# Kernel optimization log

Measured on AMD Instinct MI355X. Metric: run time of the kernel, lower is better.

## Reference

```python
import jax, jax.numpy as jnp
import numpy as np

N, E = 50000, 800000
F_IN, H, C = 128, 8, 32  # hidden=256, heads=8 -> C=32
DROP_P = 0.6


def setup_inputs() -> dict:
    key = jax.random.key(0)
    ks = jax.random.split(key, 8)
    x = jax.random.normal(ks[0], (N, F_IN), dtype=jnp.float32)
    edge_index = jax.random.randint(ks[1], (2, E), 0, N, dtype=jnp.int64)
    # precomputed inverted-dropout masks (Bernoulli keep * 1/(1-p)), as passed via dp_mask args
    dp_mask = (jax.random.uniform(ks[2], (E, H)) > DROP_P).astype(jnp.float32) / (1.0 - DROP_P)
    dp_mask_self = (jax.random.uniform(ks[3], (N, H)) > DROP_P).astype(jnp.float32) / (1.0 - DROP_P)
    # learned parameters of GATConv
    W = jax.random.normal(ks[4], (F_IN, H * C), dtype=jnp.float32) * (1.0 / np.sqrt(F_IN))
    att_src = jax.random.normal(ks[5], (H, C), dtype=jnp.float32) * 0.1
    att_dst = jax.random.normal(ks[6], (H, C), dtype=jnp.float32) * 0.1
    bias = jnp.zeros((H * C,), dtype=jnp.float32)
    return {"x": x, "edge_index": edge_index, "dp_mask": dp_mask,
            "dp_mask_self": dp_mask_self, "W": W, "att_src": att_src,
            "att_dst": att_dst, "bias": bias}


def reference(x, edge_index, dp_mask, dp_mask_self, W, att_src, att_dst, bias):
    n = x.shape[0]
    h = (x @ W).reshape(n, H, C)                      # [N,H,C]
    a_src = jnp.sum(h * att_src, axis=-1)             # [N,H] source-side score
    a_dst = jnp.sum(h * att_dst, axis=-1)             # [N,H] dest-side score
    # flow='target_to_source': aggregate at edge_index[0], gather from edge_index[1]
    dst = edge_index[0]
    src = edge_index[1]
    e_alpha = jax.nn.leaky_relu(a_src[src] + a_dst[dst], 0.2)   # [E,H]
    s_alpha = jax.nn.leaky_relu(a_src + a_dst, 0.2)             # [N,H] self-loops
    seg = jnp.concatenate([dst, jnp.arange(n, dtype=dst.dtype)])
    alpha = jnp.concatenate([e_alpha, s_alpha], axis=0)         # [E+N,H]
    # segment softmax over each destination's neighborhood (incl. self-loop)
    m = jax.ops.segment_max(alpha, seg, num_segments=n)
    ex = jnp.exp(alpha - m[seg])
    denom = jax.ops.segment_sum(ex, seg, num_segments=n)
    p = ex / denom[seg]                                         # [E+N,H]
    # dropout on attention coefficients (masks passed in)
    p = p * jnp.concatenate([dp_mask, dp_mask_self], axis=0)
    msgs = jnp.concatenate([h[src], h], axis=0)                 # [E+N,H,C]
    out = jax.ops.segment_sum(p[:, :, None] * msgs, seg, num_segments=n)
    return out.reshape(n, H * C) + bias                         # concat heads + bias
```

## Files before the change

### kernel.cpp

```cpp
#include <hip/hip_runtime.h>

#define NN 50000
#define FIN 128
#define HC 256
#define NH 8
#define NE 800000
#define WROW 136
#define GEMMB 782
#define NBLK1 3907
#define OVFCAP 131072

typedef __attribute__((ext_vector_type(8))) short short8;
typedef __attribute__((ext_vector_type(4))) short short4v;
typedef __attribute__((ext_vector_type(4))) float floatx4;

__device__ __forceinline__ float bf2f(unsigned short u) {
    union { unsigned int i; float f; } v; v.i = ((unsigned int)u) << 16; return v.f;
}
__device__ __forceinline__ unsigned short f2bf(float f) {
    union { float f; unsigned int i; } v; v.f = f;
    unsigned int r = v.i + 0x7fffu + ((v.i >> 16) & 1u);
    return (unsigned short)(r >> 16);
}
__device__ __forceinline__ float lrelu(float x) { return x > 0.f ? x : 0.2f * x; }
__device__ __forceinline__ float ldf(const void* p, int f32, long long i) {
    return f32 ? ((const float*)p)[i] : bf2f(((const unsigned short*)p)[i]);
}
__device__ __forceinline__ int lde(const int* ei, int i64, long long i) {
    return i64 ? (int)((const long long*)ei)[i] : ei[i];
}
__device__ __forceinline__ float sel8(const float s[2][4], int t2, int rr) {
    float a0 = t2 ? s[1][0] : s[0][0];
    float a1 = t2 ? s[1][1] : s[0][1];
    float a2 = t2 ? s[1][2] : s[0][2];
    float a3 = t2 ? s[1][3] : s[0][3];
    return (rr == 0) ? a0 : ((rr == 1) ? a1 : ((rr == 2) ? a2 : a3));
}
__device__ __forceinline__ float blo(unsigned int u) {
    union { unsigned int i; float f; } v; v.i = u << 16; return v.f;
}
__device__ __forceinline__ float bhi(unsigned int u) {
    union { unsigned int i; float f; } v; v.i = u & 0xFFFF0000u; return v.f;
}
__device__ __forceinline__ float bperm(int addr, float v) {
    return __uint_as_float((unsigned int)__builtin_amdgcn_ds_bpermute(addr, (int)__float_as_uint(v)));
}

__global__ __launch_bounds__(256) void k_front(
        const void* __restrict__ x, const int* __restrict__ ei,
        const void* __restrict__ dpm, const void* __restrict__ W,
        const void* __restrict__ as_, const void* __restrict__ ad_,
        int* __restrict__ flags, unsigned short* __restrict__ h,
        float* __restrict__ a_src, float* __restrict__ a_dst,
        int* __restrict__ cnt, int* __restrict__ ovfcnt,
        unsigned int* __restrict__ bucket, int2* __restrict__ ovf, int cap) {
    __shared__ unsigned short lwt[128 * WROW];
    __shared__ int s_bad, s_nz;
    const int tid = threadIdx.x;
    const int b = blockIdx.x;

    if (tid == 0) { s_bad = 0; s_nz = 0; }
    __syncthreads();
    {
        unsigned int wv = ((const unsigned int*)dpm)[tid];
        if (wv != 0u && wv != 0x40200000u) atomicAdd(&s_bad, 1);
        if (((const unsigned int*)ei)[2 * tid + 1] != 0u) atomicAdd(&s_nz, 1);
    }
    __syncthreads();
    const int f32 = (s_bad == 0) ? 1 : 0;
    const int i64 = (s_nz == 0) ? 1 : 0;
    if (b == 0 && tid == 0) { flags[0] = f32; flags[1] = i64; }

    if (b < GEMMB) {
        const int ch = b & 1;
        const int rb = b >> 1;
        {
            const int lcol = tid & 127;
            const int col = ch * 128 + lcol;
            const int k0 = (tid >> 7) * 64;
            if (f32) {
                const float* wp = (const float*)W + col;
                for (int k = k0; k < k0 + 64; k++) lwt[lcol * WROW + k] = f2bf(wp[(long long)k * HC]);
            } else {
                const unsigned short* wp = (const unsigned short*)W + col;
                for (int k = k0; k < k0 + 64; k++) lwt[lcol * WROW + k] = wp[(long long)k * HC];
            }
        }
        __syncthreads();

        const int lane = tid & 63;
        const int wave = tid >> 6;
        const int lrow = lane & 15;
        const int quad = lane >> 4;
        const int row0w = rb * 128 + wave * 32;

        short8 a[2][4];
        #pragma unroll
        for (int t = 0; t < 2; t++)
            #pragma unroll
            for (int q = 0; q < 4; q++)
                #pragma unroll
                for (int j = 0; j < 8; j++) a[t][q][j] = 0;

        #pragma unroll
        for (int t = 0; t < 2; t++) {
            int row = row0w + t * 16 + lrow;
            if (row < NN) {
                if (f32) {
                    const float* xp = (const float*)x + (long long)row * FIN + quad * 8;
                    #pragma unroll
                    for (int q = 0; q < 4; q++) {
                        floatx4 u0 = *(const floatx4*)(xp + q * 32);
                        floatx4 u1 = *(const floatx4*)(xp + q * 32 + 4);
                        #pragma unroll
                        for (int j = 0; j < 4; j++) {
                            a[t][q][j]     = (short)f2bf(u0[j]);
                            a[t][q][j + 4] = (short)f2bf(u1[j]);
                        }
                    }
                } else {
                    const unsigned short* xp = (const unsigned short*)x + (long long)row * FIN + quad * 8;
                    #pragma unroll
                    for (int q = 0; q < 4; q++) a[t][q] = *(const short8*)(xp + q * 32);
                }
            }
        }

        float sS[2][4], sD[2][4];
        #pragma unroll 4
        for (int ct = 0; ct < 8; ct++) {
            if ((ct & 1) == 0) {
                #pragma unroll
                for (int t = 0; t < 2; t++)
                    #pragma unroll
                    for (int r = 0; r < 4; r++) { sS[t][r] = 0.f; sD[t][r] = 0.f; }
            }
            floatx4 acc0 = {0.f, 0.f, 0.f, 0.f};
            floatx4 acc1 = {0.f, 0.f, 0.f, 0.f};
            const unsigned short* wp = lwt + (ct * 16 + lrow) * WROW + quad * 8;
            #pragma unroll
            for (int q = 0; q < 4; q++) {
                short8 bb = *(const short8*)(wp + q * 32);
                acc0 = __builtin_amdgcn_mfma_f32_16x16x32_bf16(a[0][q], bb, acc0, 0, 0, 0);
                acc1 = __builtin_amdgcn_mfma_f32_16x16x32_bf16(a[1][q], bb, acc1, 0, 0, 0);
            }
            const int gcol = ch * 128 + ct * 16 + lrow;
            #pragma unroll
            for (int r = 0; r < 4; r++) {
                int orow = row0w + quad * 4 + r;
                if (orow < NN) h[(long long)orow * HC + gcol] = f2bf(acc0[r]);
                int orow1 = orow + 16;
                if (orow1 < NN) h[(long long)orow1 * HC + gcol] = f2bf(acc1[r]);
            }
            float tS = ldf(as_, f32, gcol);
            float tD = ldf(ad_, f32, gcol);
            #pragma unroll
            for (int r = 0; r < 4; r++) {
                sS[0][r] += acc0[r] * tS;  sS[1][r] += acc1[r] * tS;
                sD[0][r] += acc0[r] * tD;  sD[1][r] += acc1[r] * tD;
            }
            if (ct & 1) {
                #pragma unroll
                for (int m = 1; m <= 8; m <<= 1)
                    #pragma unroll
                    for (int t = 0; t < 2; t++)
                        #pragma unroll
                        for (int r = 0; r < 4; r++) {
                            sS[t][r] += __shfl_xor(sS[t][r], m);
                            sD[t][r] += __shfl_xor(sD[t][r], m);
                        }
                int hd = ch * 4 + (ct >> 1);
                if (lrow < 8) {
                    int t2 = lrow >> 2, rr = lrow & 3;
                    int row = row0w + t2 * 16 + quad * 4 + rr;
                    if (row < NN) a_src[row * NH + hd] = sel8(sS, t2, rr);
                } else {
                    int lr = lrow - 8;
                    int t2 = lr >> 2, rr = lr & 3;
                    int row = row0w + t2 * 16 + quad * 4 + rr;
                    if (row < NN) a_dst[row * NH + hd] = sel8(sD, t2, rr);
                }
            }
        }
    } else {
        int e = (b - GEMMB) * 256 + tid;
        int dst = lde(ei, i64, e);
        int src = lde(ei, i64, (long long)NE + e);
        unsigned int msk = 0;
        if (f32) {
            const floatx4* dp = (const floatx4*)((const float*)dpm + (long long)e * 8);
            floatx4 d0 = dp[0], d1 = dp[1];
            #pragma unroll
            for (int j = 0; j < 4; j++) {
                msk |= (d0[j] != 0.f ? 1u : 0u) << j;
                msk |= (d1[j] != 0.f ? 1u : 0u) << (4 + j);
            }
        } else {
            short8 dd = *(const short8*)((const unsigned short*)dpm + (long long)e * 8);
            #pragma unroll
            for (int j = 0; j < 8; j++) msk |= (dd[j] != 0 ? 1u : 0u) << j;
        }
        unsigned int entry = (unsigned int)src | (msk << 16);
        int pos = atomicAdd(&cnt[dst], 1);
        if (pos < cap) bucket[(long long)dst * cap + pos] = entry;
        else {
            int op = atomicAdd(ovfcnt, 1);
            if (op < OVFCAP) ovf[op] = make_int2(dst, (int)entry);
        }
    }
}

__global__ __launch_bounds__(256) void k_aggr(
        const int* __restrict__ cnt, const int* __restrict__ ovfcnt,
        const unsigned int* __restrict__ bucket, const int2* __restrict__ ovf,
        const float* __restrict__ a_src, const float* __restrict__ a_dst,
        const unsigned short* __restrict__ h, const void* __restrict__ dps,
        const int* __restrict__ flags, const void* __restrict__ bs_,
        void* __restrict__ out, int cap) {
    int node = blockIdx.x * 4 + (threadIdx.x >> 6);
    int lane = threadIdx.x & 63;
    if (node >= NN) return;
    const int unode = __builtin_amdgcn_readfirstlane(node);
    const int f32 = flags[0];
    int novf = *ovfcnt; novf = novf > OVFCAP ? OVFCAP : novf;
    int mn = cnt[unode]; mn = mn < cap ? mn : cap;
    const unsigned int* __restrict__ bp = bucket + (long long)unode * cap;

    const int hh = lane >> 3;
    const int e8 = lane & 7;
    const int badr = (lane & 56) << 2;
    const int cb = lane * 4;
    const float adst = a_dst[unode * NH + hh];

    float dnp = 0.f;
    float acc0 = 0.f, acc1 = 0.f, acc2 = 0.f, acc3 = 0.f;

    for (int j = 0; j < mn; j += 8) {
        unsigned int u0 = bp[j + 0], u1 = bp[j + 1], u2 = bp[j + 2], u3 = bp[j + 3],
                     u4 = bp[j + 4], u5 = bp[j + 5], u6 = bp[j + 6], u7 = bp[j + 7];

        int idx = j + e8;
        int idxc = idx < mn ? idx : mn - 1;
        unsigned int ue = bp[idxc];
        int esrc = (int)(ue & 0xFFFFu);
        float al = a_src[esrc * NH + hh] + adst;
        float w = __expf(fmaxf(al, 0.2f * al));
        w = idx < mn ? w : 0.f;
        dnp += w;
        float ws = ((ue >> (16 + hh)) & 1u) ? w : -w;

        #define GATW(K) float w##K = bperm(badr + 4 * K, ws);
        GATW(0) GATW(1) GATW(2) GATW(3) GATW(4) GATW(5) GATW(6) GATW(7)
        #undef GATW

        #define GATH(K) \
            const unsigned short* hp##K = h + \
                (((long long)(__builtin_amdgcn_readfirstlane((int)u##K) & 0xFFFF)) << 8); \
            uint2 v##K = make_uint2(0u, 0u); \
            if (w##K > 0.f) v##K = *(const uint2*)(hp##K + cb);
        GATH(0) GATH(1) GATH(2) GATH(3) GATH(4) GATH(5) GATH(6) GATH(7)
        #undef GATH

        #define MACC(K) { float p = w##K * 2.5f; \
            acc0 = fmaf(p, blo(v##K.x), acc0); acc1 = fmaf(p, bhi(v##K.x), acc1); \
            acc2 = fmaf(p, blo(v##K.y), acc2); acc3 = fmaf(p, bhi(v##K.y), acc3); }
        MACC(0) MACC(1) MACC(2) MACC(3) MACC(4) MACC(5) MACC(6) MACC(7)
        #undef MACC
    }

    dnp += __shfl_xor(dnp, 1);
    dnp += __shfl_xor(dnp, 2);
    dnp += __shfl_xor(dnp, 4);
    float dn = dnp;

    for (int i = 0; i < novf; i++) {
        int2 tv = ovf[i];
        if (tv.x == node) {
            unsigned int u = (unsigned int)tv.y;
            int src = (int)(u & 0xFFFFu);
            float w = __expf(lrelu(a_src[src * NH + hh] + adst));
            dn += w;
            if ((u >> (16 + hh)) & 1u) {
                uint2 hv = *(const uint2*)(h + ((long long)src << 8) + cb);
                float p = w * 2.5f;
                acc0 = fmaf(p, blo(hv.x), acc0); acc1 = fmaf(p, bhi(hv.x), acc1);
                acc2 = fmaf(p, blo(hv.y), acc2); acc3 = fmaf(p, bhi(hv.y), acc3);
            }
        }
    }
    {
        float wS = __expf(lrelu(a_src[unode * NH + hh] + adst));
        dn += wS;
        float pS = wS * ldf(dps, f32, (long long)unode * NH + hh);
        uint2 hv = *(const uint2*)(h + ((long long)unode << 8) + cb);
        acc0 = fmaf(pS, blo(hv.x), acc0); acc1 = fmaf(pS, bhi(hv.x), acc1);
        acc2 = fmaf(pS, blo(hv.y), acc2); acc3 = fmaf(pS, bhi(hv.y), acc3);
    }
    float inv = 1.0f / dn;
    float b0 = ldf(bs_, f32, cb + 0), b1 = ldf(bs_, f32, cb + 1);
    float b2 = ldf(bs_, f32, cb + 2), b3 = ldf(bs_, f32, cb + 3);
    if (f32) {
        floatx4 o = {acc0 * inv + b0, acc1 * inv + b1, acc2 * inv + b2, acc3 * inv + b3};
        *(floatx4*)((float*)out + (long long)node * HC + cb) = o;
    } else {
        short4v o;
        o[0] = (short)f2bf(acc0 * inv + b0);
        o[1] = (short)f2bf(acc1 * inv + b1);
        o[2] = (short)f2bf(acc2 * inv + b2);
        o[3] = (short)f2bf(acc3 * inv + b3);
        *(short4v*)((unsigned short*)out + (long long)node * HC + cb) = o;
    }
}

extern "C" void kernel_launch(void* const* d_in, const int* in_sizes, int n_in,
                              void* d_out, int out_size, void* d_ws, size_t ws_size,
                              hipStream_t stream) {
    const void* x       = d_in[0];
    const int*  ei      = (const int*)d_in[1];
    const void* dp_mask = d_in[2];
    const void* dp_self = d_in[3];
    const void* W       = d_in[4];
    const void* att_s   = d_in[5];
    const void* att_d   = d_in[6];
    const void* bias    = d_in[7];

    char* w = (char*)d_ws;
    unsigned short* h      = (unsigned short*)(w + 0);
    float*          a_src  = (float*)(w + 25600000);
    float*          a_dst  = (float*)(w + 27200000);
    int*            cnt    = (int*)(w + 28800000);
    int*            ovfcnt = (int*)(w + 29000000);
    int*            flags  = (int*)(w + 29000064);
    int2*           ovf    = (int2*)(w + 29000960);
    unsigned int*   bucket = (unsigned int*)(w + 30049536);

    long long avail = (long long)ws_size - 30049536LL - 256LL;
    int cap = (int)(avail / 200000LL);
    if (cap > 64) cap = 64;
    if (cap < 4) cap = 4;

    hipMemsetAsync(cnt, 0, 200960, stream);
    k_front<<<NBLK1, 256, 0, stream>>>(x, ei, dp_mask, W, att_s, att_d,
                                       flags, h, a_src, a_dst, cnt, ovfcnt, bucket, ovf, cap);
    k_aggr<<<NN / 4, 256, 0, stream>>>(cnt, ovfcnt, bucket, ovf, a_src, a_dst, h,
                                       dp_self, flags, bias, d_out, cap);
}
```

Baseline: 216.5 us.

## Pad edge counters, batch edge fill per block, and hoist neighbor gathers

Edge bucketing moves to the first 782 blocks, each handling 1024 edges, so the fill overlaps the GEMM blocks scheduled after it. Per-node counters are spaced 16 ints apart so atomics on nearby nodes no longer share a cache line. The bucket capacity becomes a power of two so indexing uses shifts. In aggregation, the eight row gathers are issued unconditionally before the weight computation, and each lane's entry is selected from registers instead of a second bucket load. This gives more memory parallelism at the cost of fetching rows that dropout will mask out.

Result: slower. 236.6 us (+9.3%).

```diff
diff --git a/kernel.cpp b/kernel.cpp
--- a/kernel.cpp
+++ b/kernel.cpp
@@ -6,9 +6,11 @@
 #define NH 8
 #define NE 800000
 #define WROW 136
+#define FILLB 782
 #define GEMMB 782
-#define NBLK1 3907
+#define NBLK1 1564
 #define OVFCAP 131072
+#define CSTR 16
 
 typedef __attribute__((ext_vector_type(8))) short short8;
 typedef __attribute__((ext_vector_type(4))) short short4v;
@@ -53,7 +55,8 @@
         int* __restrict__ flags, unsigned short* __restrict__ h,
         float* __restrict__ a_src, float* __restrict__ a_dst,
         int* __restrict__ cnt, int* __restrict__ ovfcnt,
-        unsigned int* __restrict__ bucket, int2* __restrict__ ovf, int cap) {
+        unsigned int* __restrict__ bucket, int2* __restrict__ ovf,
+        int cap, int capl2) {
     __shared__ unsigned short lwt[128 * WROW];
     __shared__ int s_bad, s_nz;
     const int tid = threadIdx.x;
@@ -71,9 +74,41 @@
     const int i64 = (s_nz == 0) ? 1 : 0;
     if (b == 0 && tid == 0) { flags[0] = f32; flags[1] = i64; }
 
-    if (b < GEMMB) {
-        const int ch = b & 1;
-        const int rb = b >> 1;
+    if (b < FILLB) {
+        const long long e0 = (long long)b * 1024 + tid;
+        #pragma unroll
+        for (int i = 0; i < 4; i++) {
+            long long e = e0 + i * 256;
+            if (e < NE) {
+                int dst = lde(ei, i64, e);
+                int src = lde(ei, i64, (long long)NE + e);
+                unsigned int msk = 0;
+                if (f32) {
+                    const floatx4* dp = (const floatx4*)((const float*)dpm + e * 8);
+                    floatx4 d0 = dp[0], d1 = dp[1];
+                    #pragma unroll
+                    for (int j = 0; j < 4; j++) {
+                        msk |= (d0[j] != 0.f ? 1u : 0u) << j;
+                        msk |= (d1[j] != 0.f ? 1u : 0u) << (4 + j);
+                    }
+                } else {
+                    short8 dd = *(const short8*)((const unsigned short*)dpm + e * 8);
+                    #pragma unroll
+                    for (int j = 0; j < 8; j++) msk |= (dd[j] != 0 ? 1u : 0u) << j;
+                }
+                unsigned int entry = (unsigned int)src | (msk << 16);
+                int pos = atomicAdd(&cnt[dst * CSTR], 1);
+                if (pos < cap) bucket[((long long)dst << capl2) + pos] = entry;
+                else {
+                    int op = atomicAdd(ovfcnt, 1);
+                    if (op < OVFCAP) ovf[op] = make_int2(dst, (int)entry);
+                }
+            }
+        }
+    } else {
+        const int bb = b - FILLB;
+        const int ch = bb & 1;
+        const int rb = bb >> 1;
         {
             const int lcol = tid & 127;
             const int col = ch * 128 + lcol;
@@ -140,9 +175,9 @@
             const unsigned short* wp = lwt + (ct * 16 + lrow) * WROW + quad * 8;
             #pragma unroll
             for (int q = 0; q < 4; q++) {
-                short8 bb = *(const short8*)(wp + q * 32);
-                acc0 = __builtin_amdgcn_mfma_f32_16x16x32_bf16(a[0][q], bb, acc0, 0, 0, 0);
-                acc1 = __builtin_amdgcn_mfma_f32_16x16x32_bf16(a[1][q], bb, acc1, 0, 0, 0);
+                short8 bb2 = *(const short8*)(wp + q * 32);
+                acc0 = __builtin_amdgcn_mfma_f32_16x16x32_bf16(a[0][q], bb2, acc0, 0, 0, 0);
+                acc1 = __builtin_amdgcn_mfma_f32_16x16x32_bf16(a[1][q], bb2, acc1, 0, 0, 0);
             }
             const int gcol = ch * 128 + ct * 16 + lrow;
             #pragma unroll
@@ -182,31 +217,6 @@
                 }
             }
         }
-    } else {
-        int e = (b - GEMMB) * 256 + tid;
-        int dst = lde(ei, i64, e);
-        int src = lde(ei, i64, (long long)NE + e);
-        unsigned int msk = 0;
-        if (f32) {
-            const floatx4* dp = (const floatx4*)((const float*)dpm + (long long)e * 8);
-            floatx4 d0 = dp[0], d1 = dp[1];
-            #pragma unroll
-            for (int j = 0; j < 4; j++) {
-                msk |= (d0[j] != 0.f ? 1u : 0u) << j;
-                msk |= (d1[j] != 0.f ? 1u : 0u) << (4 + j);
-            }
-        } else {
-            short8 dd = *(const short8*)((const unsigned short*)dpm + (long long)e * 8);
-            #pragma unroll
-            for (int j = 0; j < 8; j++) msk |= (dd[j] != 0 ? 1u : 0u) << j;
-        }
-        unsigned int entry = (unsigned int)src | (msk << 16);
-        int pos = atomicAdd(&cnt[dst], 1);
-        if (pos < cap) bucket[(long long)dst * cap + pos] = entry;
-        else {
-            int op = atomicAdd(ovfcnt, 1);
-            if (op < OVFCAP) ovf[op] = make_int2(dst, (int)entry);
-        }
     }
 }
 
@@ -216,15 +226,15 @@
         const float* __restrict__ a_src, const float* __restrict__ a_dst,
         const unsigned short* __restrict__ h, const void* __restrict__ dps,
         const int* __restrict__ flags, const void* __restrict__ bs_,
-        void* __restrict__ out, int cap) {
+        void* __restrict__ out, int cap, int capl2) {
     int node = blockIdx.x * 4 + (threadIdx.x >> 6);
     int lane = threadIdx.x & 63;
     if (node >= NN) return;
     const int unode = __builtin_amdgcn_readfirstlane(node);
     const int f32 = flags[0];
     int novf = *ovfcnt; novf = novf > OVFCAP ? OVFCAP : novf;
-    int mn = cnt[unode]; mn = mn < cap ? mn : cap;
-    const unsigned int* __restrict__ bp = bucket + (long long)unode * cap;
+    int mn = cnt[unode * CSTR]; mn = mn < cap ? mn : cap;
+    const unsigned int* __restrict__ bp = bucket + ((long long)unode << capl2);
 
     const int hh = lane >> 3;
     const int e8 = lane & 7;
@@ -239,9 +249,21 @@
         unsigned int u0 = bp[j + 0], u1 = bp[j + 1], u2 = bp[j + 2], u3 = bp[j + 3],
                      u4 = bp[j + 4], u5 = bp[j + 5], u6 = bp[j + 6], u7 = bp[j + 7];
 
+        #define GATH(K) \
+            const unsigned short* hp##K = h + \
+                (((long long)(__builtin_amdgcn_readfirstlane((int)u##K) & 0xFFFF)) << 8); \
+            uint2 v##K = *(const uint2*)(hp##K + cb);
+        GATH(0) GATH(1) GATH(2) GATH(3) GATH(4) GATH(5) GATH(6) GATH(7)
+        #undef GATH
+
+        unsigned int s0a = (e8 & 1) ? u1 : u0;
+        unsigned int s1a = (e8 & 1) ? u3 : u2;
+        unsigned int s2a = (e8 & 1) ? u5 : u4;
+        unsigned int s3a = (e8 & 1) ? u7 : u6;
+        unsigned int t0a = (e8 & 2) ? s1a : s0a;
+        unsigned int t1a = (e8 & 2) ? s3a : s2a;
+        unsigned int ue  = (e8 & 4) ? t1a : t0a;
         int idx = j + e8;
-        int idxc = idx < mn ? idx : mn - 1;
-        unsigned int ue = bp[idxc];
         int esrc = (int)(ue & 0xFFFFu);
         float al = a_src[esrc * NH + hh] + adst;
         float w = __expf(fmaxf(al, 0.2f * al));
@@ -249,23 +271,15 @@
         dnp += w;
         float ws = ((ue >> (16 + hh)) & 1u) ? w : -w;
 
-        #define GATW(K) float w##K = bperm(badr + 4 * K, ws);
-        GATW(0) GATW(1) GATW(2) GATW(3) GATW(4) GATW(5) GATW(6) GATW(7)
-        #undef GATW
-
-        #define GATH(K) \
-            const unsigned short* hp##K = h + \
-                (((long long)(__builtin_amdgcn_readfirstlane((int)u##K) & 0xFFFF)) << 8); \
-            uint2 v##K = make_uint2(0u, 0u); \
-            if (w##K > 0.f) v##K = *(const uint2*)(hp##K + cb);
-        GATH(0) GATH(1) GATH(2) GATH(3) GATH(4) GATH(5) GATH(6) GATH(7)
-        #undef GATH
-
-        #define MACC(K) { float p = w##K * 2.5f; \
-            acc0 = fmaf(p, blo(v##K.x), acc0); acc1 = fmaf(p, bhi(v##K.x), acc1); \
-            acc2 = fmaf(p, blo(v##K.y), acc2); acc3 = fmaf(p, bhi(v##K.y), acc3); }
-        MACC(0) MACC(1) MACC(2) MACC(3) MACC(4) MACC(5) MACC(6) MACC(7)
-        #undef MACC
+        #define CONS(K) { \
+            float wv = bperm(badr + 4 * K, ws); \
+            float p = fmaxf(wv, 0.f) * 2.5f; \
+            unsigned int gx = wv > 0.f ? v##K.x : 0u; \
+            unsigned int gy = wv > 0.f ? v##K.y : 0u; \
+            acc0 = fmaf(p, blo(gx), acc0); acc1 = fmaf(p, bhi(gx), acc1); \
+            acc2 = fmaf(p, blo(gy), acc2); acc3 = fmaf(p, bhi(gy), acc3); }
+        CONS(0) CONS(1) CONS(2) CONS(3) CONS(4) CONS(5) CONS(6) CONS(7)
+        #undef CONS
     }
 
     dnp += __shfl_xor(dnp, 1);
@@ -329,19 +343,19 @@
     float*          a_src  = (float*)(w + 25600000);
     float*          a_dst  = (float*)(w + 27200000);
     int*            cnt    = (int*)(w + 28800000);
-    int*            ovfcnt = (int*)(w + 29000000);
-    int*            flags  = (int*)(w + 29000064);
-    int2*           ovf    = (int2*)(w + 29000960);
-    unsigned int*   bucket = (unsigned int*)(w + 30049536);
-
-    long long avail = (long long)ws_size - 30049536LL - 256LL;
-    int cap = (int)(avail / 200000LL);
-    if (cap > 64) cap = 64;
-    if (cap < 4) cap = 4;
-
-    hipMemsetAsync(cnt, 0, 200960, stream);
+    int*            ovfcnt = (int*)(w + 32000000);
+    int*            flags  = (int*)(w + 32000064);
+    int2*           ovf    = (int2*)(w + 32000960);
+    unsigned int*   bucket = (unsigned int*)(w + 33049536);
+
+    long long avail = (long long)ws_size - 33049536LL - 512LL;
+    int cap = 64, capl2 = 6;
+    while (cap > 4 && (long long)cap * 200000LL > avail) { cap >>= 1; capl2--; }
+
+    hipMemsetAsync(cnt, 0, 3200128, stream);
     k_front<<<NBLK1, 256, 0, stream>>>(x, ei, dp_mask, W, att_s, att_d,
-                                       flags, h, a_src, a_dst, cnt, ovfcnt, bucket, ovf, cap);
+                                       flags, h, a_src, a_dst, cnt, ovfcnt, bucket, ovf,
+                                       cap, capl2);
     k_aggr<<<NN / 4, 256, 0, stream>>>(cnt, ovfcnt, bucket, ovf, a_src, a_dst, h,
-                                       dp_self, flags, bias, d_out, cap);
-}
+                                       dp_self, flags, bias, d_out, cap, capl2);
+}
```

## Split front kernel into separate edge-fill and GEMM kernels; reuse A tile across halves

Applied to the files above, without the earlier changes.

The fused front kernel, which mixed GEMM blocks and edge-bucketing blocks, becomes two kernels: k_fill scatters edges into per-destination buckets and k_gemm computes h and the attention scores. Each GEMM block now loads its x rows once and loops over both 128-column halves of W, halving the redundant x reads and bf16 conversions. The bucket capacity is rounded to a power of two so addressing uses shifts. In exchange the GEMM and the atomic-heavy fill no longer run concurrently, there is an extra launch, and the smaller bucket cap may push more edges into the overflow list.

Measured after the change: 230.0 us. +6.3%, slower.

```diff
diff --git a/kernel.cpp b/kernel.cpp
--- a/kernel.cpp
+++ b/kernel.cpp
@@ -6,8 +6,8 @@
 #define NH 8
 #define NE 800000
 #define WROW 136
-#define GEMMB 782
-#define NBLK1 3907
+#define FILLB 3125
+#define GEMMB 391
 #define OVFCAP 131072
 
 typedef __attribute__((ext_vector_type(8))) short short8;
@@ -46,19 +46,14 @@
     return __uint_as_float((unsigned int)__builtin_amdgcn_ds_bpermute(addr, (int)__float_as_uint(v)));
 }
 
-__global__ __launch_bounds__(256) void k_front(
-        const void* __restrict__ x, const int* __restrict__ ei,
-        const void* __restrict__ dpm, const void* __restrict__ W,
-        const void* __restrict__ as_, const void* __restrict__ ad_,
-        int* __restrict__ flags, unsigned short* __restrict__ h,
-        float* __restrict__ a_src, float* __restrict__ a_dst,
-        int* __restrict__ cnt, int* __restrict__ ovfcnt,
-        unsigned int* __restrict__ bucket, int2* __restrict__ ovf, int cap) {
-    __shared__ unsigned short lwt[128 * WROW];
+__global__ __launch_bounds__(256) void k_fill(
+        const int* __restrict__ ei, const void* __restrict__ dpm,
+        int* __restrict__ flags, int* __restrict__ cnt, int* __restrict__ ovfcnt,
+        unsigned int* __restrict__ bucket, int2* __restrict__ ovf,
+        int cap, int capl2) {
     __shared__ int s_bad, s_nz;
     const int tid = threadIdx.x;
     const int b = blockIdx.x;
-
     if (tid == 0) { s_bad = 0; s_nz = 0; }
     __syncthreads();
     {
@@ -71,9 +66,92 @@
     const int i64 = (s_nz == 0) ? 1 : 0;
     if (b == 0 && tid == 0) { flags[0] = f32; flags[1] = i64; }
 
-    if (b < GEMMB) {
-        const int ch = b & 1;
-        const int rb = b >> 1;
+    const long long e = (long long)b * 256 + tid;
+    int dst = lde(ei, i64, e);
+    int src = lde(ei, i64, (long long)NE + e);
+    unsigned int msk = 0;
+    if (f32) {
+        const floatx4* dp = (const floatx4*)((const float*)dpm + e * 8);
+        floatx4 d0 = dp[0], d1 = dp[1];
+        #pragma unroll
+        for (int j = 0; j < 4; j++) {
+            msk |= (d0[j] != 0.f ? 1u : 0u) << j;
+            msk |= (d1[j] != 0.f ? 1u : 0u) << (4 + j);
+        }
+    } else {
+        short8 dd = *(const short8*)((const unsigned short*)dpm + e * 8);
+        #pragma unroll
+        for (int j = 0; j < 8; j++) msk |= (dd[j] != 0 ? 1u : 0u) << j;
+    }
+    unsigned int entry = (unsigned int)src | (msk << 16);
+    int pos = atomicAdd(&cnt[dst], 1);
+    if (pos < cap) bucket[((long long)dst << capl2) + pos] = entry;
+    else {
+        int op = atomicAdd(ovfcnt, 1);
+        if (op < OVFCAP) ovf[op] = make_int2(dst, (int)entry);
+    }
+}
+
+__global__ __launch_bounds__(256) void k_gemm(
+        const void* __restrict__ x, const void* __restrict__ dpm,
+        const void* __restrict__ W,
+        const void* __restrict__ as_, const void* __restrict__ ad_,
+        unsigned short* __restrict__ h,
+        float* __restrict__ a_src, float* __restrict__ a_dst) {
+    __shared__ unsigned short lwt[128 * WROW];
+    __shared__ int s_bad;
+    const int tid = threadIdx.x;
+    const int b = blockIdx.x;
+    if (tid == 0) s_bad = 0;
+    __syncthreads();
+    {
+        unsigned int wv = ((const unsigned int*)dpm)[tid];
+        if (wv != 0u && wv != 0x40200000u) atomicAdd(&s_bad, 1);
+    }
+    __syncthreads();
+    const int f32 = (s_bad == 0) ? 1 : 0;
+
+    const int lane = tid & 63;
+    const int wave = tid >> 6;
+    const int lrow = lane & 15;
+    const int quad = lane >> 4;
+    const int row0w = b * 128 + wave * 32;
+
+    short8 a[2][4];
+    #pragma unroll
+    for (int t = 0; t < 2; t++)
+        #pragma unroll
+        for (int q = 0; q < 4; q++)
+            #pragma unroll
+            for (int j = 0; j < 8; j++) a[t][q][j] = 0;
+
+    #pragma unroll
+    for (int t = 0; t < 2; t++) {
+        int row = row0w + t * 16 + lrow;
+        if (row < NN) {
+            if (f32) {
+                const float* xp = (const float*)x + (long long)row * FIN + quad * 8;
+                #pragma unroll
+                for (int q = 0; q < 4; q++) {
+                    floatx4 u0 = *(const floatx4*)(xp + q * 32);
+                    floatx4 u1 = *(const floatx4*)(xp + q * 32 + 4);
+                    #pragma unroll
+                    for (int j = 0; j < 4; j++) {
+                        a[t][q][j]     = (short)f2bf(u0[j]);
+                        a[t][q][j + 4] = (short)f2bf(u1[j]);
+                    }
+                }
+            } else {
+                const unsigned short* xp = (const unsigned short*)x + (long long)row * FIN + quad * 8;
+                #pragma unroll
+                for (int q = 0; q < 4; q++) a[t][q] = *(const short8*)(xp + q * 32);
+            }
+        }
+    }
+
+    #pragma unroll
+    for (int ch = 0; ch < 2; ch++) {
+        if (ch) __syncthreads();
         {
             const int lcol = tid & 127;
             const int col = ch * 128 + lcol;
@@ -87,44 +165,6 @@
             }
         }
         __syncthreads();
-
-        const int lane = tid & 63;
-        const int wave = tid >> 6;
-        const int lrow = lane & 15;
-        const int quad = lane >> 4;
-        const int row0w = rb * 128 + wave * 32;
-
-        short8 a[2][4];
-        #pragma unroll
-        for (int t = 0; t < 2; t++)
-            #pragma unroll
-            for (int q = 0; q < 4; q++)
-                #pragma unroll
-                for (int j = 0; j < 8; j++) a[t][q][j] = 0;
-
-        #pragma unroll
-        for (int t = 0; t < 2; t++) {
-            int row = row0w + t * 16 + lrow;
-            if (row < NN) {
-                if (f32) {
-                    const float* xp = (const float*)x + (long long)row * FIN + quad * 8;
-                    #pragma unroll
-                    for (int q = 0; q < 4; q++) {
-                        floatx4 u0 = *(const floatx4*)(xp + q * 32);
-                        floatx4 u1 = *(const floatx4*)(xp + q * 32 + 4);
-                        #pragma unroll
-                        for (int j = 0; j < 4; j++) {
-                            a[t][q][j]     = (short)f2bf(u0[j]);
-                            a[t][q][j + 4] = (short)f2bf(u1[j]);
-                        }
-                    }
-                } else {
-                    const unsigned short* xp = (const unsigned short*)x + (long long)row * FIN + quad * 8;
-                    #pragma unroll
-                    for (int q = 0; q < 4; q++) a[t][q] = *(const short8*)(xp + q * 32);
-                }
-            }
-        }
 
         float sS[2][4], sD[2][4];
         #pragma unroll 4
@@ -182,31 +222,6 @@
                 }
             }
         }
-    } else {
-        int e = (b - GEMMB) * 256 + tid;
-        int dst = lde(ei, i64, e);
-        int src = lde(ei, i64, (long long)NE + e);
-        unsigned int msk = 0;
-        if (f32) {
-            const floatx4* dp = (const floatx4*)((const float*)dpm + (long long)e * 8);
-            floatx4 d0 = dp[0], d1 = dp[1];
-            #pragma unroll
-            for (int j = 0; j < 4; j++) {
-                msk |= (d0[j] != 0.f ? 1u : 0u) << j;
-                msk |= (d1[j] != 0.f ? 1u : 0u) << (4 + j);
-            }
-        } else {
-            short8 dd = *(const short8*)((const unsigned short*)dpm + (long long)e * 8);
-            #pragma unroll
-            for (int j = 0; j < 8; j++) msk |= (dd[j] != 0 ? 1u : 0u) << j;
-        }
-        unsigned int entry = (unsigned int)src | (msk << 16);
-        int pos = atomicAdd(&cnt[dst], 1);
-        if (pos < cap) bucket[(long long)dst * cap + pos] = entry;
-        else {
-            int op = atomicAdd(ovfcnt, 1);
-            if (op < OVFCAP) ovf[op] = make_int2(dst, (int)entry);
-        }
     }
 }
 
@@ -216,7 +231,7 @@
         const float* __restrict__ a_src, const float* __restrict__ a_dst,
         const unsigned short* __restrict__ h, const void* __restrict__ dps,
         const int* __restrict__ flags, const void* __restrict__ bs_,
-        void* __restrict__ out, int cap) {
+        void* __restrict__ out, int cap, int capl2) {
     int node = blockIdx.x * 4 + (threadIdx.x >> 6);
     int lane = threadIdx.x & 63;
     if (node >= NN) return;
@@ -224,7 +239,7 @@
     const int f32 = flags[0];
     int novf = *ovfcnt; novf = novf > OVFCAP ? OVFCAP : novf;
     int mn = cnt[unode]; mn = mn < cap ? mn : cap;
-    const unsigned int* __restrict__ bp = bucket + (long long)unode * cap;
+    const unsigned int* __restrict__ bp = bucket + ((long long)unode << capl2);
 
     const int hh = lane >> 3;
     const int e8 = lane & 7;
@@ -334,14 +349,14 @@
     int2*           ovf    = (int2*)(w + 29000960);
     unsigned int*   bucket = (unsigned int*)(w + 30049536);
 
-    long long avail = (long long)ws_size - 30049536LL - 256LL;
-    int cap = (int)(avail / 200000LL);
-    if (cap > 64) cap = 64;
-    if (cap < 4) cap = 4;
+    long long avail = (long long)ws_size - 30049536LL - 512LL;
+    int cap = 64, capl2 = 6;
+    while (cap > 4 && (long long)cap * 200000LL > avail) { cap >>= 1; capl2--; }
 
     hipMemsetAsync(cnt, 0, 200960, stream);
-    k_front<<<NBLK1, 256, 0, stream>>>(x, ei, dp_mask, W, att_s, att_d,
-                                       flags, h, a_src, a_dst, cnt, ovfcnt, bucket, ovf, cap);
+    k_fill<<<FILLB, 256, 0, stream>>>(ei, dp_mask, flags, cnt, ovfcnt, bucket, ovf,
+                                      cap, capl2);
+    k_gemm<<<GEMMB, 256, 0, stream>>>(x, dp_mask, W, att_s, att_d, h, a_src, a_dst);
     k_aggr<<<NN / 4, 256, 0, stream>>>(cnt, ovfcnt, bucket, ovf, a_src, a_dst, h,
-                                       dp_self, flags, bias, d_out, cap);
-}
+                                       dp_self, flags, bias, d_out, cap, capl2);
+}
```
